# Kernel tuning notes

Hardware: AMD Instinct MI355X
Metric: run time of the kernel (lower is better)

The kernel has to match this reference:

```python
import jax, jax.numpy as jnp
import numpy as np

N, K, D, DOUT = 100000, 16, 128, 128

def setup_inputs() -> dict:
    key = jax.random.key(0)
    k1, k2, k3 = jax.random.split(key, 3)
    self_vecs = jax.random.normal(k1, (N, D), dtype=jnp.float32)
    neigh_vecs = jax.random.normal(k2, (N, K, D), dtype=jnp.float32)
    # glorot([input_dim, output_dim])
    limit = np.sqrt(6.0 / (D + DOUT)).astype(np.float32)
    weights = jax.random.uniform(k3, (D, DOUT), dtype=jnp.float32, minval=-limit, maxval=limit)
    return {"self_vecs": self_vecs, "neigh_vecs": neigh_vecs, "weights": weights}

def reference(self_vecs, neigh_vecs, weights):
    # concat self node as an extra "neighbor": [N, K+1, D]
    neigh_self = jnp.concatenate([neigh_vecs, self_vecs[:, None, :]], axis=1)
    # attention scores: query is the self vector, keys are neighbors+self -> [N, K+1]
    score = jnp.einsum('nd,nkd->nk', self_vecs, neigh_self)
    attn = jax.nn.softmax(score, axis=-1)
    # weighted sum of values -> [N, D]
    context = jnp.einsum('nk,nkd->nd', attn, neigh_self)
    out = context @ weights  # [N, DOUT]
    return jax.nn.relu(out)
```

## Files before the change

kernel.cpp:

```cpp
#include <hip/hip_runtime.h>


constexpr int K    = 16;
constexpr int D    = 128;
constexpr int DOUT = 128;
constexpr int WT_PITCH = 136;

typedef short bfrag  __attribute__((ext_vector_type(8)));
typedef float afrag  __attribute__((ext_vector_type(4)));

__device__ __forceinline__ unsigned short f2bf(float f) {
    union { float f; unsigned u; } v; v.f = f;
    const unsigned r = v.u + 0x7FFF + ((v.u >> 16) & 1);
    return (unsigned short)(r >> 16);
}
__device__ __forceinline__ float bf2f(unsigned short b) {
    union { unsigned u; float f; } v; v.u = ((unsigned)b) << 16;
    return v.f;
}

__device__ __forceinline__ float half_allsum(float x) {
    #pragma unroll
    for (int off = 1; off <= 16; off <<= 1)
        x += __shfl_xor(x, off);
    return x;
}

__launch_bounds__(512, 2)
__global__ void gat_fused(const float* __restrict__ self_vecs,
                          const float* __restrict__ neigh_vecs,
                          const float* __restrict__ W,
                          float* __restrict__ out,
                          int n_tiles) {
    __shared__ __align__(16) unsigned short Wt[DOUT][WT_PITCH];
    __shared__ __align__(16) unsigned short Chl[2][2][16][WT_PITCH];

    const int tid = threadIdx.x;

    for (int e = tid; e < D * DOUT; e += blockDim.x) {
        const int k = e >> 7, m = e & 127;
        Wt[m][k] = f2bf(W[e]);
    }
    __syncthreads();

    const int lane = tid & 63;
    const int wid  = tid >> 6;
    const int half = lane >> 5;
    const int q    = lane & 31;
    const int nl   = lane & 15;
    const int kb   = lane >> 4;
    const int r0   = wid * 2;

    float4 v[K], sv;

    int buf = 0;
    int t = blockIdx.x;

    if (t < n_tiles) {
        const int n0 = t * 16 + r0 + half;
        const float4* nb = (const float4*)(neigh_vecs + (size_t)n0 * (K * D)) + q;
        #pragma unroll
        for (int k = 0; k < K; ++k) v[k] = nb[k * 32];
        sv = ((const float4*)(self_vecs + (size_t)n0 * D))[q];
    }

    for (; t < n_tiles; t += gridDim.x, buf ^= 1) {
        const int node0 = t * 16;

        float ss = sv.x * sv.x + sv.y * sv.y + sv.z * sv.z + sv.w * sv.w;
        float sc[K];
        #pragma unroll
        for (int k = 0; k < K; ++k)
            sc[k] = sv.x * v[k].x + sv.y * v[k].y + sv.z * v[k].z + sv.w * v[k].w;
        ss = half_allsum(ss);
        #pragma unroll
        for (int k = 0; k < K; ++k) sc[k] = half_allsum(sc[k]);

        float m = ss;
        #pragma unroll
        for (int k = 0; k < K; ++k) m = fmaxf(m, sc[k]);
        float e   = __expf(ss - m);
        float sum = e;
        float4 cx = make_float4(e * sv.x, e * sv.y, e * sv.z, e * sv.w);
        #pragma unroll
        for (int k = 0; k < K; ++k) {
            const float ek = __expf(sc[k] - m);
            sum += ek;
            cx.x += ek * v[k].x; cx.y += ek * v[k].y;
            cx.z += ek * v[k].z; cx.w += ek * v[k].w;
        }
        const float inv = 1.f / sum;
        const float cf[4] = {cx.x * inv, cx.y * inv, cx.z * inv, cx.w * inv};

        unsigned short hi4[4], lo4[4];
        #pragma unroll
        for (int i = 0; i < 4; ++i) {
            hi4[i] = f2bf(cf[i]);
            lo4[i] = f2bf(cf[i] - bf2f(hi4[i]));
        }
        *(uint2*)&Chl[buf][0][r0 + half][4 * q] = *(const uint2*)hi4;
        *(uint2*)&Chl[buf][1][r0 + half][4 * q] = *(const uint2*)lo4;

        __syncthreads();

        const int tn = t + gridDim.x;
        if (tn < n_tiles) {
            const int n0 = tn * 16 + r0 + half;
            const float4* nb = (const float4*)(neigh_vecs + (size_t)n0 * (K * D)) + q;
            #pragma unroll
            for (int k = 0; k < K; ++k) v[k] = nb[k * 32];
            sv = ((const float4*)(self_vecs + (size_t)n0 * D))[q];
        }

        afrag acc;
        #pragma unroll
        for (int r4 = 0; r4 < 4; ++r4) acc[r4] = 0.f;

        #pragma unroll
        for (int kc = 0; kc < 4; ++kc) {
            const bfrag ch = *(const bfrag*)&Chl[buf][0][nl][kc * 32 + kb * 8];
            const bfrag cl = *(const bfrag*)&Chl[buf][1][nl][kc * 32 + kb * 8];
            const bfrag a  = *(const bfrag*)&Wt[wid * 16 + nl][kc * 32 + kb * 8];
            acc = __builtin_amdgcn_mfma_f32_16x16x32_bf16(a, ch, acc, 0, 0, 0);
            acc = __builtin_amdgcn_mfma_f32_16x16x32_bf16(a, cl, acc, 0, 0, 0);
        }
        float* orow = out + (size_t)(node0 + nl) * DOUT + kb * 4;
        *(float4*)(orow + wid * 16) =
            make_float4(fmaxf(acc[0], 0.f), fmaxf(acc[1], 0.f),
                        fmaxf(acc[2], 0.f), fmaxf(acc[3], 0.f));
    }
}

extern "C" void kernel_launch(void* const* d_in, const int* in_sizes, int n_in,
                              void* d_out, int out_size, void* d_ws, size_t ws_size,
                              hipStream_t stream) {
    const float* self_vecs = (const float*)d_in[0];
    const float* neigh     = (const float*)d_in[1];
    const float* W         = (const float*)d_in[2];
    float* out = (float*)d_out;

    const int n_nodes = in_sizes[0] / D;
    const int n_tiles = n_nodes / 16;

    const int tpb = 512;
    const int blocks = 512;
    gat_fused<<<dim3(blocks), dim3(tpb), 0, stream>>>(
        self_vecs, neigh, W, out, n_tiles);
}
```

Baseline: 190.8 us.

## Issue next-tile neighbor loads per register during softmax and shift by self-score

Result: no change. 190.0 us (-0.4%).

```diff
diff --git a/kernel.cpp b/kernel.cpp
--- a/kernel.cpp
+++ b/kernel.cpp
@@ -66,29 +66,26 @@
 
     for (; t < n_tiles; t += gridDim.x, buf ^= 1) {
         const int node0 = t * 16;
+        const int tn  = t + gridDim.x;
+        const int tl  = (tn < n_tiles) ? tn : t;
+        const int nn0 = tl * 16 + r0 + half;
+        const float4* nbN = (const float4*)(neigh_vecs + (size_t)nn0 * (K * D)) + q;
 
-        float ss = sv.x * sv.x + sv.y * sv.y + sv.z * sv.z + sv.w * sv.w;
-        float sc[K];
-        #pragma unroll
-        for (int k = 0; k < K; ++k)
-            sc[k] = sv.x * v[k].x + sv.y * v[k].y + sv.z * v[k].z + sv.w * v[k].w;
-        ss = half_allsum(ss);
-        #pragma unroll
-        for (int k = 0; k < K; ++k) sc[k] = half_allsum(sc[k]);
-
-        float m = ss;
-        #pragma unroll
-        for (int k = 0; k < K; ++k) m = fmaxf(m, sc[k]);
-        float e   = __expf(ss - m);
-        float sum = e;
-        float4 cx = make_float4(e * sv.x, e * sv.y, e * sv.z, e * sv.w);
+        float ss = half_allsum(sv.x * sv.x + sv.y * sv.y + sv.z * sv.z + sv.w * sv.w);
+        float sum = 1.f;
+        float4 cx = sv;
         #pragma unroll
         for (int k = 0; k < K; ++k) {
-            const float ek = __expf(sc[k] - m);
-            sum += ek;
-            cx.x += ek * v[k].x; cx.y += ek * v[k].y;
-            cx.z += ek * v[k].z; cx.w += ek * v[k].w;
+            float p = sv.x * v[k].x + sv.y * v[k].y + sv.z * v[k].z + sv.w * v[k].w;
+            p = half_allsum(p);
+            const float e = __expf(p - ss);
+            sum += e;
+            cx.x += e * v[k].x; cx.y += e * v[k].y;
+            cx.z += e * v[k].z; cx.w += e * v[k].w;
+            v[k] = nbN[k * 32];
         }
+        sv = ((const float4*)(self_vecs + (size_t)nn0 * D))[q];
+
         const float inv = 1.f / sum;
         const float cf[4] = {cx.x * inv, cx.y * inv, cx.z * inv, cx.w * inv};
 
@@ -102,15 +99,6 @@
         *(uint2*)&Chl[buf][1][r0 + half][4 * q] = *(const uint2*)lo4;
 
         __syncthreads();
-
-        const int tn = t + gridDim.x;
-        if (tn < n_tiles) {
-            const int n0 = tn * 16 + r0 + half;
-            const float4* nb = (const float4*)(neigh_vecs + (size_t)n0 * (K * D)) + q;
-            #pragma unroll
-            for (int k = 0; k < K; ++k) v[k] = nb[k * 32];
-            sv = ((const float4*)(self_vecs + (size_t)n0 * D))[q];
-        }
 
         afrag acc;
         #pragma unroll
```
